# Kernel optimization log

Hardware: AMD Instinct MI355X
Metric: run time of the kernel (lower is better)

The kernel has to match this reference:

```python
import jax, jax.numpy as jnp
import numpy as np

B, N, D = 128, 512, 64
DELTA_BEARING = 30.0
DELTA_HEADING = 30.0
DOMAIN_PARAM = 5.0
NB_H = int(360 // DELTA_HEADING)  # 12
NB_B = int(360 // DELTA_BEARING)  # 12
EPS = 1e-14


def setup_inputs() -> dict:
    key = jax.random.key(0)
    k1, k2, k3, k4, k5 = jax.random.split(key, 5)
    hidden_state = jax.random.normal(k1, (B, N, D), dtype=jnp.float32)
    distance_matrix = jax.random.uniform(k2, (B, N, N), dtype=jnp.float32) * 10.0
    bearing_matrix = jax.random.uniform(k3, (B, N, N), dtype=jnp.float32) * 360.0
    heading_matrix = jax.random.uniform(k4, (B, N, N), dtype=jnp.float32) * 360.0
    sequence_mask = (jax.random.uniform(k5, (B, N)) > 0.1).astype(jnp.float32)
    domain = jnp.full((NB_H, NB_B), DOMAIN_PARAM, dtype=jnp.float32)
    return {
        "hidden_state": hidden_state,
        "distance_matrix": distance_matrix,
        "bearing_matrix": bearing_matrix,
        "heading_matrix": heading_matrix,
        "sequence_mask": sequence_mask,
        "domain": domain,
    }


def _convert_to_bins(bearing, heading):
    sh = heading + DELTA_HEADING / 2
    sb = bearing + DELTA_BEARING / 2
    sh = jnp.where(sh >= 360.0, sh - 360.0, sh)
    sb = jnp.where(sb >= 360.0, sb - 360.0, sb)
    idx1 = jnp.clip(jnp.floor(sh / DELTA_HEADING), 0, NB_H - 1).astype(jnp.int32)
    idx2 = jnp.clip(jnp.floor(sb / DELTA_BEARING), 0, NB_B - 1).astype(jnp.int32)
    return idx1, idx2


def _compute_weights(distance, bearing, heading, seq_mask, domain):
    n = distance.shape[1]
    idx1, idx2 = _convert_to_bins(bearing, heading)
    # gather domain bins, relu threshold against distance
    w = jax.nn.relu(domain[idx1, idx2] - distance)  # (B,N,N)
    # pairwise validity mask, zero diagonal (self-pedestrian)
    wm = seq_mask[:, :, None] * seq_mask[:, None, :]
    self_ped = 1.0 - jnp.eye(n, dtype=w.dtype)
    m = wm * self_ped
    w = w * m
    # max-normalize along neighbors
    w = w / (jnp.max(w, axis=2, keepdims=True) + EPS)
    w = w * m
    # masked softmax over dim=2 (mask = nonzero entries)
    nz = (w != 0).astype(w.dtype)
    exps = jnp.exp(w) * nz
    sums = jnp.sum(exps, axis=2, keepdims=True)
    w = jnp.where(sums != 0, exps / (sums + EPS), jnp.zeros_like(exps))
    w = w * m
    return w


def reference(hidden_state, distance_matrix, bearing_matrix, heading_matrix, sequence_mask, domain):
    b, n, d = hidden_state.shape
    weights = _compute_weights(distance_matrix, bearing_matrix, heading_matrix, sequence_mask, domain)
    weighted_hidden = jnp.einsum("bij,bjd->bid", weights, hidden_state)
    weighted_hidden = weighted_hidden.reshape(b * n, d)
    return jnp.concatenate([weighted_hidden, hidden_state.reshape(b * n, d)], axis=1)
```

## Files before the change

### kernel.cpp

```cpp
#include <hip/hip_runtime.h>
#include <hip/hip_fp16.h>

typedef float    f32x4 __attribute__((ext_vector_type(4)));
typedef _Float16 f16x8 __attribute__((ext_vector_type(8)));
typedef _Float16 f16x4 __attribute__((ext_vector_type(4)));

#define NBB   512
#define HT_ST 520

__device__ __forceinline__ int binidx(float heading, float bearing) {
    float sh = heading + 15.0f; sh = (sh >= 360.0f) ? sh - 360.0f : sh;
    float sb = bearing + 15.0f; sb = (sb >= 360.0f) ? sb - 360.0f : sb;
    int ih = (int)floorf(sh * (1.0f / 30.0f)); ih = min(max(ih, 0), 11);
    int ib = (int)floorf(sb * (1.0f / 30.0f)); ib = min(max(ib, 0), 11);
    return ih * 12 + ib;
}

__global__ __launch_bounds__(512, 4) void spatial_attn_kernel(
    const float* __restrict__ hid,
    const float* __restrict__ dist,
    const float* __restrict__ bear,
    const float* __restrict__ head,
    const float* __restrict__ mask,
    const float* __restrict__ dom,
    float* __restrict__ out)
{
    __shared__ __align__(16) _Float16 sHT[64][HT_ST];
    __shared__ __align__(16) float    sMask[NBB];
    __shared__ __align__(16) float    sDom[144];

    const int tid  = threadIdx.x;
    const int lane = tid & 63;
    const int wid  = tid >> 6;
    const int l16  = lane & 15;
    const int kg   = lane >> 4;

    const int g    = blockIdx.x;
    const int xcd  = g & 7;
    const int jj8  = g >> 3;
    const int b    = xcd * 16 + (jj8 >> 2);
    const int i0blk = (jj8 & 3) << 7;

    if (tid < NBB) sMask[tid] = mask[b * NBB + tid];
    if (tid < 144) sDom[tid]  = dom[tid];

    {
        const int d4 = tid & 15;
        const int jg = tid >> 4;
        const f32x4* hid4 = (const f32x4*)(hid + (size_t)b * NBB * 64);
        #pragma unroll
        for (int it = 0; it < 4; ++it) {
            const int j0 = 4 * jg + 128 * it;
            f32x4 v0 = hid4[(j0 + 0) * 16 + d4];
            f32x4 v1 = hid4[(j0 + 1) * 16 + d4];
            f32x4 v2 = hid4[(j0 + 2) * 16 + d4];
            f32x4 v3 = hid4[(j0 + 3) * 16 + d4];
            if (j0 >= i0blk && j0 < i0blk + 128) {
                *(f32x4*)(out + (size_t)(b * NBB + j0 + 0) * 128 + 64 + 4 * d4) = v0;
                *(f32x4*)(out + (size_t)(b * NBB + j0 + 1) * 128 + 64 + 4 * d4) = v1;
                *(f32x4*)(out + (size_t)(b * NBB + j0 + 2) * 128 + 64 + 4 * d4) = v2;
                *(f32x4*)(out + (size_t)(b * NBB + j0 + 3) * 128 + 64 + 4 * d4) = v3;
            }
            #pragma unroll
            for (int c = 0; c < 4; ++c) {
                f16x4 hv;
                hv[0] = (_Float16)v0[c]; hv[1] = (_Float16)v1[c];
                hv[2] = (_Float16)v2[c]; hv[3] = (_Float16)v3[c];
                *(f16x4*)&sHT[4 * d4 + c][j0] = hv;
            }
        }
    }
    __syncthreads();

    const float domc = sDom[0];
    int okc = (sDom[lane] == domc) && (sDom[lane + 64] == domc);
    if (lane < 16) okc = okc && (sDom[lane + 128] == domc);
    const bool uni = __all(okc);

    const int   i   = i0blk + wid * 16 + l16;
    const float mi  = sMask[i];
    const float* dbase = dist + ((size_t)b * NBB + i) * NBB + 8 * kg;

    f16x8 w[16];
    float mx = 0.0f;

    if (uni) {
        f32x4 LA[4], LB[4];
        #pragma unroll
        for (int p = 0; p < 4; ++p) {
            LA[p] = *(const f32x4*)(dbase + 32 * p);
            LB[p] = *(const f32x4*)(dbase + 32 * p + 4);
        }
        #pragma unroll
        for (int t = 0; t < 16; ++t) {
            const f32x4 da = LA[t & 3];
            const f32x4 dc = LB[t & 3];
            if (t < 12) {
                LA[t & 3] = *(const f32x4*)(dbase + 32 * (t + 4));
                LB[t & 3] = *(const f32x4*)(dbase + 32 * (t + 4) + 4);
            }
            const int kbase = 32 * t + 8 * kg;
            const f32x4 m0 = *(const f32x4*)(sMask + kbase);
            const f32x4 m1 = *(const f32x4*)(sMask + kbase + 4);
            float ww[8];
            #pragma unroll
            for (int q = 0; q < 4; ++q) {
                ww[q]     = fmaxf(domc - da[q], 0.0f) * m0[q];
                ww[q + 4] = fmaxf(domc - dc[q], 0.0f) * m1[q];
            }
            if ((i >> 5) == t) {
                #pragma unroll
                for (int q = 0; q < 8; ++q)
                    if (kbase + q == i) ww[q] = 0.0f;
            }
            f16x8 h;
            #pragma unroll
            for (int q = 0; q < 8; ++q) {
                mx = fmaxf(mx, ww[q]);
                h[q] = (_Float16)ww[q];
            }
            w[t] = h;
        }
    } else {
        const float* bbase = bear + ((size_t)b * NBB + i) * NBB + 8 * kg;
        const float* hbase = head + ((size_t)b * NBB + i) * NBB + 8 * kg;
        #pragma unroll
        for (int t = 0; t < 16; ++t) {
            const f32x4 d0 = *(const f32x4*)(dbase + 32 * t);
            const f32x4 d1 = *(const f32x4*)(dbase + 32 * t + 4);
            const f32x4 b0 = *(const f32x4*)(bbase + 32 * t);
            const f32x4 b1 = *(const f32x4*)(bbase + 32 * t + 4);
            const f32x4 h0 = *(const f32x4*)(hbase + 32 * t);
            const f32x4 h1 = *(const f32x4*)(hbase + 32 * t + 4);
            const int kbase = 32 * t + 8 * kg;
            const f32x4 m0 = *(const f32x4*)(sMask + kbase);
            const f32x4 m1 = *(const f32x4*)(sMask + kbase + 4);
            float ww[8];
            #pragma unroll
            for (int q = 0; q < 4; ++q) {
                ww[q]     = fmaxf(sDom[binidx(h0[q], b0[q])] - d0[q], 0.0f) * m0[q];
                ww[q + 4] = fmaxf(sDom[binidx(h1[q], b1[q])] - d1[q], 0.0f) * m1[q];
            }
            if ((i >> 5) == t) {
                #pragma unroll
                for (int q = 0; q < 8; ++q)
                    if (kbase + q == i) ww[q] = 0.0f;
            }
            f16x8 h;
            #pragma unroll
            for (int q = 0; q < 8; ++q) {
                mx = fmaxf(mx, ww[q]);
                h[q] = (_Float16)ww[q];
            }
            w[t] = h;
        }
    }

    mx = fmaxf(mx, __shfl_xor(mx, 16));
    mx = fmaxf(mx, __shfl_xor(mx, 32));
    const float rinv = 1.0f / (mx + 1e-14f);

    float s = 0.0f;
    #pragma unroll
    for (int t = 0; t < 16; ++t) {
        f16x8 h = w[t];
        #pragma unroll
        for (int q = 0; q < 8; ++q) {
            const float wn = (float)h[q] * rinv;
            const float e  = (wn != 0.0f) ? __expf(wn) : 0.0f;
            s += e;
            h[q] = (_Float16)e;
        }
        w[t] = h;
    }
    s += __shfl_xor(s, 16);
    s += __shfl_xor(s, 32);
    const float gsc = (s != 0.0f) ? (mi / (s + 1e-14f)) : 0.0f;

    f32x4 acc0 = {0.f,0.f,0.f,0.f}, acc1 = acc0, acc2 = acc0, acc3 = acc0;
    #pragma unroll
    for (int t = 0; t < 16; ++t) {
        const f16x8 bf = w[t];
        const int col = 32 * t + 8 * kg;
        acc0 = __builtin_amdgcn_mfma_f32_16x16x32_f16(*(const f16x8*)&sHT[     l16][col], bf, acc0, 0, 0, 0);
        acc1 = __builtin_amdgcn_mfma_f32_16x16x32_f16(*(const f16x8*)&sHT[16 + l16][col], bf, acc1, 0, 0, 0);
        acc2 = __builtin_amdgcn_mfma_f32_16x16x32_f16(*(const f16x8*)&sHT[32 + l16][col], bf, acc2, 0, 0, 0);
        acc3 = __builtin_amdgcn_mfma_f32_16x16x32_f16(*(const f16x8*)&sHT[48 + l16][col], bf, acc3, 0, 0, 0);
    }

    float* orow = out + ((size_t)b * NBB + i) * 128 + 4 * kg;
    *(f32x4*)(orow +  0) = acc0 * gsc;
    *(f32x4*)(orow + 16) = acc1 * gsc;
    *(f32x4*)(orow + 32) = acc2 * gsc;
    *(f32x4*)(orow + 48) = acc3 * gsc;
}

extern "C" void kernel_launch(void* const* d_in, const int* in_sizes, int n_in,
                              void* d_out, int out_size, void* d_ws, size_t ws_size,
                              hipStream_t stream) {
    (void)in_sizes; (void)n_in; (void)d_ws; (void)ws_size; (void)out_size;
    const float* hid  = (const float*)d_in[0];
    const float* dist = (const float*)d_in[1];
    const float* bear = (const float*)d_in[2];
    const float* head = (const float*)d_in[3];
    const float* mask = (const float*)d_in[4];
    const float* dom  = (const float*)d_in[5];
    float* out = (float*)d_out;
    hipLaunchKernelGGL(spatial_attn_kernel, dim3(512), dim3(512), 0, stream,
                       hid, dist, bear, head, mask, dom, out);
}
```

Measured before the change: 339.8 us.

## Recompute weights in two passes to drop register-held weight tiles

Instead of keeping all 16 f16x8 weight tiles in registers across the max, exp and MFMA phases, the kernel now makes a first pass over the distance row to compute the max, then re-reads the distances in a second pass that fuses exp, sum and the MFMA accumulation. This lowers register pressure and may allow higher occupancy. The cost is reading the distance matrix twice from global memory or cache, and dropping the explicit software prefetch. The non-uniform path is restructured the same way with partial unrolling.

```diff
diff --git a/kernel.cpp b/kernel.cpp
--- a/kernel.cpp
+++ b/kernel.cpp
@@ -77,54 +77,91 @@
     if (lane < 16) okc = okc && (sDom[lane + 128] == domc);
     const bool uni = __all(okc);
 
-    const int   i   = i0blk + wid * 16 + l16;
-    const float mi  = sMask[i];
-    const float* dbase = dist + ((size_t)b * NBB + i) * NBB + 8 * kg;
-
-    f16x8 w[16];
-    float mx = 0.0f;
+    const int    i     = i0blk + wid * 16 + l16;
+    const float  mi    = sMask[i];
+    const size_t gri   = (size_t)b * NBB + i;
+    const float* dbase = dist + gri * NBB + 8 * kg;
+    const int    tdiag = i >> 5;
+
+    f32x4 acc0 = {0.f,0.f,0.f,0.f}, acc1 = acc0, acc2 = acc0, acc3 = acc0;
+    float sum;
 
     if (uni) {
-        f32x4 LA[4], LB[4];
+        f32x4 mxA = acc0, mxB = acc0;
         #pragma unroll
-        for (int p = 0; p < 4; ++p) {
-            LA[p] = *(const f32x4*)(dbase + 32 * p);
-            LB[p] = *(const f32x4*)(dbase + 32 * p + 4);
-        }
+        for (int t = 0; t < 16; ++t) {
+            const f32x4 d0 = *(const f32x4*)(dbase + 32 * t);
+            const f32x4 d1 = *(const f32x4*)(dbase + 32 * t + 4);
+            const int kbase = 32 * t + 8 * kg;
+            const f32x4 m0 = *(const f32x4*)(sMask + kbase);
+            const f32x4 m1 = *(const f32x4*)(sMask + kbase + 4);
+            f32x4 wA, wB;
+            #pragma unroll
+            for (int q = 0; q < 4; ++q) {
+                wA[q] = fmaxf(domc - d0[q], 0.0f) * m0[q];
+                wB[q] = fmaxf(domc - d1[q], 0.0f) * m1[q];
+            }
+            if (t == tdiag) {
+                #pragma unroll
+                for (int q = 0; q < 4; ++q) {
+                    if (kbase + q     == i) wA[q] = 0.0f;
+                    if (kbase + 4 + q == i) wB[q] = 0.0f;
+                }
+            }
+            #pragma unroll
+            for (int q = 0; q < 4; ++q) {
+                mxA[q] = fmaxf(mxA[q], wA[q]);
+                mxB[q] = fmaxf(mxB[q], wB[q]);
+            }
+        }
+        float mx = fmaxf(fmaxf(fmaxf(mxA[0], mxA[1]), fmaxf(mxA[2], mxA[3])),
+                         fmaxf(fmaxf(mxB[0], mxB[1]), fmaxf(mxB[2], mxB[3])));
+        mx = fmaxf(mx, __shfl_xor(mx, 16));
+        mx = fmaxf(mx, __shfl_xor(mx, 32));
+        const float rinv = 1.0f / (mx + 1e-14f);
+
+        f32x4 sA = acc0, sB = acc0;
         #pragma unroll
         for (int t = 0; t < 16; ++t) {
-            const f32x4 da = LA[t & 3];
-            const f32x4 dc = LB[t & 3];
-            if (t < 12) {
-                LA[t & 3] = *(const f32x4*)(dbase + 32 * (t + 4));
-                LB[t & 3] = *(const f32x4*)(dbase + 32 * (t + 4) + 4);
-            }
-            const int kbase = 32 * t + 8 * kg;
-            const f32x4 m0 = *(const f32x4*)(sMask + kbase);
-            const f32x4 m1 = *(const f32x4*)(sMask + kbase + 4);
-            float ww[8];
-            #pragma unroll
-            for (int q = 0; q < 4; ++q) {
-                ww[q]     = fmaxf(domc - da[q], 0.0f) * m0[q];
-                ww[q + 4] = fmaxf(domc - dc[q], 0.0f) * m1[q];
-            }
-            if ((i >> 5) == t) {
+            const f32x4 d0 = *(const f32x4*)(dbase + 32 * t);
+            const f32x4 d1 = *(const f32x4*)(dbase + 32 * t + 4);
+            const int kbase = 32 * t + 8 * kg;
+            const f32x4 m0 = *(const f32x4*)(sMask + kbase);
+            const f32x4 m1 = *(const f32x4*)(sMask + kbase + 4);
+            f32x4 wA, wB;
+            #pragma unroll
+            for (int q = 0; q < 4; ++q) {
+                wA[q] = fmaxf(domc - d0[q], 0.0f) * m0[q];
+                wB[q] = fmaxf(domc - d1[q], 0.0f) * m1[q];
+            }
+            if (t == tdiag) {
                 #pragma unroll
-                for (int q = 0; q < 8; ++q)
-                    if (kbase + q == i) ww[q] = 0.0f;
+                for (int q = 0; q < 4; ++q) {
+                    if (kbase + q     == i) wA[q] = 0.0f;
+                    if (kbase + 4 + q == i) wB[q] = 0.0f;
+                }
             }
             f16x8 h;
             #pragma unroll
-            for (int q = 0; q < 8; ++q) {
-                mx = fmaxf(mx, ww[q]);
-                h[q] = (_Float16)ww[q];
-            }
-            w[t] = h;
-        }
+            for (int q = 0; q < 4; ++q) {
+                float wn = wA[q] * rinv;
+                float e  = (wn != 0.0f) ? __expf(wn) : 0.0f;
+                sA[q] += e;  h[q] = (_Float16)e;
+                wn = wB[q] * rinv;
+                e  = (wn != 0.0f) ? __expf(wn) : 0.0f;
+                sB[q] += e;  h[4 + q] = (_Float16)e;
+            }
+            acc0 = __builtin_amdgcn_mfma_f32_16x16x32_f16(*(const f16x8*)&sHT[     l16][kbase], h, acc0, 0, 0, 0);
+            acc1 = __builtin_amdgcn_mfma_f32_16x16x32_f16(*(const f16x8*)&sHT[16 + l16][kbase], h, acc1, 0, 0, 0);
+            acc2 = __builtin_amdgcn_mfma_f32_16x16x32_f16(*(const f16x8*)&sHT[32 + l16][kbase], h, acc2, 0, 0, 0);
+            acc3 = __builtin_amdgcn_mfma_f32_16x16x32_f16(*(const f16x8*)&sHT[48 + l16][kbase], h, acc3, 0, 0, 0);
+        }
+        sum = sA[0]+sA[1]+sA[2]+sA[3] + sB[0]+sB[1]+sB[2]+sB[3];
     } else {
-        const float* bbase = bear + ((size_t)b * NBB + i) * NBB + 8 * kg;
-        const float* hbase = head + ((size_t)b * NBB + i) * NBB + 8 * kg;
-        #pragma unroll
+        const float* bbase = bear + gri * NBB + 8 * kg;
+        const float* hbase = head + gri * NBB + 8 * kg;
+        float mx = 0.0f;
+        #pragma unroll 2
         for (int t = 0; t < 16; ++t) {
             const f32x4 d0 = *(const f32x4*)(dbase + 32 * t);
             const f32x4 d1 = *(const f32x4*)(dbase + 32 * t + 4);
@@ -135,60 +172,57 @@
             const int kbase = 32 * t + 8 * kg;
             const f32x4 m0 = *(const f32x4*)(sMask + kbase);
             const f32x4 m1 = *(const f32x4*)(sMask + kbase + 4);
-            float ww[8];
-            #pragma unroll
-            for (int q = 0; q < 4; ++q) {
-                ww[q]     = fmaxf(sDom[binidx(h0[q], b0[q])] - d0[q], 0.0f) * m0[q];
-                ww[q + 4] = fmaxf(sDom[binidx(h1[q], b1[q])] - d1[q], 0.0f) * m1[q];
-            }
-            if ((i >> 5) == t) {
-                #pragma unroll
-                for (int q = 0; q < 8; ++q)
-                    if (kbase + q == i) ww[q] = 0.0f;
-            }
+            #pragma unroll
+            for (int q = 0; q < 4; ++q) {
+                float wA = fmaxf(sDom[binidx(h0[q], b0[q])] - d0[q], 0.0f) * m0[q];
+                float wB = fmaxf(sDom[binidx(h1[q], b1[q])] - d1[q], 0.0f) * m1[q];
+                if (kbase + q     == i) wA = 0.0f;
+                if (kbase + 4 + q == i) wB = 0.0f;
+                mx = fmaxf(mx, fmaxf(wA, wB));
+            }
+        }
+        mx = fmaxf(mx, __shfl_xor(mx, 16));
+        mx = fmaxf(mx, __shfl_xor(mx, 32));
+        const float rinv = 1.0f / (mx + 1e-14f);
+        float s = 0.0f;
+        #pragma unroll 2
+        for (int t = 0; t < 16; ++t) {
+            const f32x4 d0 = *(const f32x4*)(dbase + 32 * t);
+            const f32x4 d1 = *(const f32x4*)(dbase + 32 * t + 4);
+            const f32x4 b0 = *(const f32x4*)(bbase + 32 * t);
+            const f32x4 b1 = *(const f32x4*)(bbase + 32 * t + 4);
+            const f32x4 h0 = *(const f32x4*)(hbase + 32 * t);
+            const f32x4 h1 = *(const f32x4*)(hbase + 32 * t + 4);
+            const int kbase = 32 * t + 8 * kg;
+            const f32x4 m0 = *(const f32x4*)(sMask + kbase);
+            const f32x4 m1 = *(const f32x4*)(sMask + kbase + 4);
             f16x8 h;
             #pragma unroll
-            for (int q = 0; q < 8; ++q) {
-                mx = fmaxf(mx, ww[q]);
-                h[q] = (_Float16)ww[q];
-            }
-            w[t] = h;
-        }
+            for (int q = 0; q < 4; ++q) {
+                float wA = fmaxf(sDom[binidx(h0[q], b0[q])] - d0[q], 0.0f) * m0[q];
+                float wB = fmaxf(sDom[binidx(h1[q], b1[q])] - d1[q], 0.0f) * m1[q];
+                if (kbase + q     == i) wA = 0.0f;
+                if (kbase + 4 + q == i) wB = 0.0f;
+                float wn = wA * rinv;
+                float e  = (wn != 0.0f) ? __expf(wn) : 0.0f;
+                s += e;  h[q] = (_Float16)e;
+                wn = wB * rinv;
+                e  = (wn != 0.0f) ? __expf(wn) : 0.0f;
+                s += e;  h[4 + q] = (_Float16)e;
+            }
+            acc0 = __builtin_amdgcn_mfma_f32_16x16x32_f16(*(const f16x8*)&sHT[     l16][kbase], h, acc0, 0, 0, 0);
+            acc1 = __builtin_amdgcn_mfma_f32_16x16x32_f16(*(const f16x8*)&sHT[16 + l16][kbase], h, acc1, 0, 0, 0);
+            acc2 = __builtin_amdgcn_mfma_f32_16x16x32_f16(*(const f16x8*)&sHT[32 + l16][kbase], h, acc2, 0, 0, 0);
+            acc3 = __builtin_amdgcn_mfma_f32_16x16x32_f16(*(const f16x8*)&sHT[48 + l16][kbase], h, acc3, 0, 0, 0);
+        }
+        sum = s;
     }
 
-    mx = fmaxf(mx, __shfl_xor(mx, 16));
-    mx = fmaxf(mx, __shfl_xor(mx, 32));
-    const float rinv = 1.0f / (mx + 1e-14f);
-
-    float s = 0.0f;
-    #pragma unroll
-    for (int t = 0; t < 16; ++t) {
-        f16x8 h = w[t];
-        #pragma unroll
-        for (int q = 0; q < 8; ++q) {
-            const float wn = (float)h[q] * rinv;
-            const float e  = (wn != 0.0f) ? __expf(wn) : 0.0f;
-            s += e;
-            h[q] = (_Float16)e;
-        }
-        w[t] = h;
-    }
-    s += __shfl_xor(s, 16);
-    s += __shfl_xor(s, 32);
-    const float gsc = (s != 0.0f) ? (mi / (s + 1e-14f)) : 0.0f;
-
-    f32x4 acc0 = {0.f,0.f,0.f,0.f}, acc1 = acc0, acc2 = acc0, acc3 = acc0;
-    #pragma unroll
-    for (int t = 0; t < 16; ++t) {
-        const f16x8 bf = w[t];
-        const int col = 32 * t + 8 * kg;
-        acc0 = __builtin_amdgcn_mfma_f32_16x16x32_f16(*(const f16x8*)&sHT[     l16][col], bf, acc0, 0, 0, 0);
-        acc1 = __builtin_amdgcn_mfma_f32_16x16x32_f16(*(const f16x8*)&sHT[16 + l16][col], bf, acc1, 0, 0, 0);
-        acc2 = __builtin_amdgcn_mfma_f32_16x16x32_f16(*(const f16x8*)&sHT[32 + l16][col], bf, acc2, 0, 0, 0);
-        acc3 = __builtin_amdgcn_mfma_f32_16x16x32_f16(*(const f16x8*)&sHT[48 + l16][col], bf, acc3, 0, 0, 0);
-    }
-
-    float* orow = out + ((size_t)b * NBB + i) * 128 + 4 * kg;
+    sum += __shfl_xor(sum, 16);
+    sum += __shfl_xor(sum, 32);
+    const float gsc = (sum != 0.0f) ? (mi / (sum + 1e-14f)) : 0.0f;
+
+    float* orow = out + gri * 128 + 4 * kg;
     *(f32x4*)(orow +  0) = acc0 * gsc;
     *(f32x4*)(orow + 16) = acc1 * gsc;
     *(f32x4*)(orow + 32) = acc2 * gsc;
```

Result: slower. 405.0 us (+19.2%).
